# Performance work log

Hardware: AMD Instinct MI355X
Metric: run time of the kernel (lower is better)

Reference implementation:

```python
import jax, jax.numpy as jnp
import numpy as np

SMOOTH = 1.0

def setup_inputs() -> dict:
    key = jax.random.key(0)
    k1, k2 = jax.random.split(key)
    shape = (2, 4, 64, 256, 256)  # [B, organs, D, H, W]
    predict = jax.random.normal(k1, shape, dtype=jnp.float32)
    target = jax.random.uniform(k2, shape, dtype=jnp.float32)
    return {"predict": predict, "target": target}

def reference(predict, target):
    # sigmoid over whole prediction tensor (done once in DiceLoss.forward)
    p = jax.nn.sigmoid(predict)
    B, O, D = p.shape[0], p.shape[1], p.shape[2]
    # BinaryDiceLoss views each [D, H, W] organ slice as (D, H*W):
    pf = p.reshape(B, O, D, -1)
    tf = target.reshape(B, O, D, -1)
    num = jnp.sum(pf * tf, axis=-1)                      # [B, O, D]
    den = jnp.sum(pf, axis=-1) + jnp.sum(tf, axis=-1) + SMOOTH
    dice_loss = 1.0 - 2.0 * num / den                    # [B, O, D]
    # slices with first element == -1 are ignored
    valid = (tf[..., 0] != -1).astype(dice_loss.dtype)   # [B, O, D]
    per_slice_avg = jnp.sum(dice_loss * valid, axis=-1) / jnp.sum(valid, axis=-1)  # [B, O]
    # outer loop averages over all B*4 (b, organ) pairs
    return jnp.mean(per_slice_avg)
```

## Files before the change

kernel.cpp:

```cpp
#include <hip/hip_runtime.h>


constexpr int HW       = 256 * 256;
constexpr int NSLICE   = 2 * 4 * 64;
constexpr int NPAIR    = 2 * 4;
constexpr int THREADS  = 1024;
constexpr int ITERS    = (HW / 4) / THREADS;

__global__ __launch_bounds__(THREADS) void dice_stage1(
    const float* __restrict__ predict,
    const float* __restrict__ target,
    float* __restrict__ ws)
{
    const int slice = blockIdx.x;
    const int tid   = threadIdx.x;
    const size_t base = (size_t)slice * HW;
    const float4* __restrict__ p4 = (const float4*)(predict + base);
    const float4* __restrict__ t4 = (const float4*)(target + base);

    float s_pt = 0.f, s_p = 0.f, s_t = 0.f;
#pragma unroll
    for (int k = 0; k < ITERS; ++k) {
        float4 pv = p4[k * THREADS + tid];
        float4 tv = t4[k * THREADS + tid];
        float e0 = 1.f / (1.f + __expf(-pv.x));
        float e1 = 1.f / (1.f + __expf(-pv.y));
        float e2 = 1.f / (1.f + __expf(-pv.z));
        float e3 = 1.f / (1.f + __expf(-pv.w));
        s_pt += e0 * tv.x;  s_pt += e1 * tv.y;
        s_pt += e2 * tv.z;  s_pt += e3 * tv.w;
        s_p  += (e0 + e1) + (e2 + e3);
        s_t  += (tv.x + tv.y) + (tv.z + tv.w);
    }

#pragma unroll
    for (int off = 32; off > 0; off >>= 1) {
        s_pt += __shfl_down(s_pt, off, 64);
        s_p  += __shfl_down(s_p,  off, 64);
        s_t  += __shfl_down(s_t,  off, 64);
    }

    __shared__ float l_pt[THREADS / 64];
    __shared__ float l_p [THREADS / 64];
    __shared__ float l_t [THREADS / 64];
    const int wave = tid >> 6;
    const int lane = tid & 63;
    if (lane == 0) { l_pt[wave] = s_pt; l_p[wave] = s_p; l_t[wave] = s_t; }
    __syncthreads();

    if (tid == 0) {
        float num = 0.f, sp = 0.f, st = 0.f;
#pragma unroll
        for (int w = 0; w < THREADS / 64; ++w) {
            num += l_pt[w]; sp += l_p[w]; st += l_t[w];
        }
        float den  = sp + st + 1.0f;
        float dice = 1.0f - 2.0f * num / den;
        float valid = (target[base] != -1.0f) ? 1.0f : 0.0f;
        ws[slice]          = dice * valid;
        ws[NSLICE + slice] = valid;
    }
}

__global__ __launch_bounds__(NSLICE) void dice_stage2(
    const float* __restrict__ ws, float* __restrict__ out)
{
    const int tid = threadIdx.x;
    float dv = ws[tid];
    float v  = ws[NSLICE + tid];
#pragma unroll
    for (int off = 32; off > 0; off >>= 1) {
        dv += __shfl_down(dv, off, 64);
        v  += __shfl_down(v,  off, 64);
    }
    __shared__ float pair_avg[NPAIR];
    const int wave = tid >> 6;
    const int lane = tid & 63;
    if (lane == 0) pair_avg[wave] = dv / v;
    __syncthreads();
    if (tid == 0) {
        float s = 0.f;
#pragma unroll
        for (int w = 0; w < NPAIR; ++w) s += pair_avg[w];
        out[0] = s * (1.0f / NPAIR);
    }
}

extern "C" void kernel_launch(void* const* d_in, const int* in_sizes, int n_in,
                              void* d_out, int out_size, void* d_ws, size_t ws_size,
                              hipStream_t stream) {
    const float* predict = (const float*)d_in[0];
    const float* target  = (const float*)d_in[1];
    float* ws  = (float*)d_ws;
    float* out = (float*)d_out;

    dice_stage1<<<NSLICE, THREADS, 0, stream>>>(predict, target, ws);
    dice_stage2<<<1, NSLICE, 0, stream>>>(ws, out);
}
```

Before: 279.2 us.

## Split each slice across four blocks and software-pipeline float4 loads

Stage 1 now launches four 256-thread blocks per slice instead of one 1024-thread block. Each block writes its raw partial sums, and the dice combine plus the validity check move into stage 2. The inner loop prefetches the next batch of four float4 loads before computing the current one, and the product accumulator is split in two to shorten the dependency chain. The goal is more blocks in flight and more memory-level parallelism for a bandwidth-bound reduction. The cost is more register pressure and a slightly larger workspace to reduce in stage 2.

```diff
diff --git a/kernel.cpp b/kernel.cpp
--- a/kernel.cpp
+++ b/kernel.cpp
@@ -1,37 +1,65 @@
 #include <hip/hip_runtime.h>
 
 
-constexpr int HW       = 256 * 256;
-constexpr int NSLICE   = 2 * 4 * 64;
-constexpr int NPAIR    = 2 * 4;
-constexpr int THREADS  = 1024;
-constexpr int ITERS    = (HW / 4) / THREADS;
+constexpr int HW     = 256 * 256;
+constexpr int NSLICE = 2 * 4 * 64;
+constexpr int NPAIR  = 2 * 4;
+constexpr int T      = 256;
+constexpr int CHUNKS_PER_SLICE = 4;
+constexpr int NCHUNK = NSLICE * CHUNKS_PER_SLICE;
+constexpr int CHUNK_ELEMS = HW / CHUNKS_PER_SLICE;
+constexpr int NITER  = CHUNK_ELEMS / 4 / T;
+constexpr int BATCH  = 4;
 
-__global__ __launch_bounds__(THREADS) void dice_stage1(
+
+__global__ __launch_bounds__(T) void dice_stage1(
     const float* __restrict__ predict,
     const float* __restrict__ target,
     float* __restrict__ ws)
 {
-    const int slice = blockIdx.x;
+    const int chunk = blockIdx.x;
     const int tid   = threadIdx.x;
-    const size_t base = (size_t)slice * HW;
+    const size_t base = (size_t)chunk * CHUNK_ELEMS;
     const float4* __restrict__ p4 = (const float4*)(predict + base);
     const float4* __restrict__ t4 = (const float4*)(target + base);
 
-    float s_pt = 0.f, s_p = 0.f, s_t = 0.f;
+    float s_pt0 = 0.f, s_pt1 = 0.f, s_p = 0.f, s_t = 0.f;
+
+    float4 pv[BATCH], tv[BATCH];
 #pragma unroll
-    for (int k = 0; k < ITERS; ++k) {
-        float4 pv = p4[k * THREADS + tid];
-        float4 tv = t4[k * THREADS + tid];
-        float e0 = 1.f / (1.f + __expf(-pv.x));
-        float e1 = 1.f / (1.f + __expf(-pv.y));
-        float e2 = 1.f / (1.f + __expf(-pv.z));
-        float e3 = 1.f / (1.f + __expf(-pv.w));
-        s_pt += e0 * tv.x;  s_pt += e1 * tv.y;
-        s_pt += e2 * tv.z;  s_pt += e3 * tv.w;
-        s_p  += (e0 + e1) + (e2 + e3);
-        s_t  += (tv.x + tv.y) + (tv.z + tv.w);
+    for (int j = 0; j < BATCH; ++j) {
+        pv[j] = p4[j * T + tid];
+        tv[j] = t4[j * T + tid];
     }
+
+#pragma unroll
+    for (int k0 = 0; k0 < NITER; k0 += BATCH) {
+        float4 cp[BATCH], ct[BATCH];
+#pragma unroll
+        for (int j = 0; j < BATCH; ++j) { cp[j] = pv[j]; ct[j] = tv[j]; }
+
+        if (k0 + BATCH < NITER) {
+#pragma unroll
+            for (int j = 0; j < BATCH; ++j) {
+                pv[j] = p4[(k0 + BATCH + j) * T + tid];
+                tv[j] = t4[(k0 + BATCH + j) * T + tid];
+            }
+        }
+
+#pragma unroll
+        for (int j = 0; j < BATCH; ++j) {
+            float e0 = 1.f / (1.f + __expf(-cp[j].x));
+            float e1 = 1.f / (1.f + __expf(-cp[j].y));
+            float e2 = 1.f / (1.f + __expf(-cp[j].z));
+            float e3 = 1.f / (1.f + __expf(-cp[j].w));
+            s_pt0 += e0 * ct[j].x + e1 * ct[j].y;
+            s_pt1 += e2 * ct[j].z + e3 * ct[j].w;
+            s_p   += (e0 + e1) + (e2 + e3);
+            s_t   += (ct[j].x + ct[j].y) + (ct[j].z + ct[j].w);
+        }
+    }
+
+    float s_pt = s_pt0 + s_pt1;
 
 #pragma unroll
     for (int off = 32; off > 0; off >>= 1) {
@@ -40,49 +68,57 @@
         s_t  += __shfl_down(s_t,  off, 64);
     }
 
-    __shared__ float l_pt[THREADS / 64];
-    __shared__ float l_p [THREADS / 64];
-    __shared__ float l_t [THREADS / 64];
+    __shared__ float l_pt[T / 64], l_p[T / 64], l_t[T / 64];
     const int wave = tid >> 6;
     const int lane = tid & 63;
     if (lane == 0) { l_pt[wave] = s_pt; l_p[wave] = s_p; l_t[wave] = s_t; }
     __syncthreads();
 
     if (tid == 0) {
-        float num = 0.f, sp = 0.f, st = 0.f;
+        float a = 0.f, b = 0.f, c = 0.f;
 #pragma unroll
-        for (int w = 0; w < THREADS / 64; ++w) {
-            num += l_pt[w]; sp += l_p[w]; st += l_t[w];
-        }
-        float den  = sp + st + 1.0f;
-        float dice = 1.0f - 2.0f * num / den;
-        float valid = (target[base] != -1.0f) ? 1.0f : 0.0f;
-        ws[slice]          = dice * valid;
-        ws[NSLICE + slice] = valid;
+        for (int w = 0; w < T / 64; ++w) { a += l_pt[w]; b += l_p[w]; c += l_t[w]; }
+        ws[chunk]              = a;
+        ws[NCHUNK + chunk]     = b;
+        ws[2 * NCHUNK + chunk] = c;
     }
 }
 
 __global__ __launch_bounds__(NSLICE) void dice_stage2(
-    const float* __restrict__ ws, float* __restrict__ out)
+    const float* __restrict__ ws,
+    const float* __restrict__ target,
+    float* __restrict__ out)
 {
-    const int tid = threadIdx.x;
-    float dv = ws[tid];
-    float v  = ws[NSLICE + tid];
+    const int s = threadIdx.x;
+    float num = 0.f, sp = 0.f, st = 0.f;
+#pragma unroll
+    for (int c = 0; c < CHUNKS_PER_SLICE; ++c) {
+        const int id = s * CHUNKS_PER_SLICE + c;
+        num += ws[id];
+        sp  += ws[NCHUNK + id];
+        st  += ws[2 * NCHUNK + id];
+    }
+    float den   = sp + st + 1.0f;
+    float dice  = 1.0f - 2.0f * num / den;
+    float valid = (target[(size_t)s * HW] != -1.0f) ? 1.0f : 0.0f;
+
+    float dv = dice * valid;
+    float v  = valid;
 #pragma unroll
     for (int off = 32; off > 0; off >>= 1) {
         dv += __shfl_down(dv, off, 64);
         v  += __shfl_down(v,  off, 64);
     }
     __shared__ float pair_avg[NPAIR];
-    const int wave = tid >> 6;
-    const int lane = tid & 63;
+    const int wave = s >> 6;
+    const int lane = s & 63;
     if (lane == 0) pair_avg[wave] = dv / v;
     __syncthreads();
-    if (tid == 0) {
-        float s = 0.f;
+    if (s == 0) {
+        float acc = 0.f;
 #pragma unroll
-        for (int w = 0; w < NPAIR; ++w) s += pair_avg[w];
-        out[0] = s * (1.0f / NPAIR);
+        for (int w = 0; w < NPAIR; ++w) acc += pair_avg[w];
+        out[0] = acc * (1.0f / NPAIR);
     }
 }
 
@@ -94,6 +130,6 @@
     float* ws  = (float*)d_ws;
     float* out = (float*)d_out;
 
-    dice_stage1<<<NSLICE, THREADS, 0, stream>>>(predict, target, ws);
-    dice_stage2<<<1, NSLICE, 0, stream>>>(ws, out);
+    dice_stage1<<<NCHUNK, T, 0, stream>>>(predict, target, ws);
+    dice_stage2<<<1, NSLICE, 0, stream>>>(ws, target, out);
 }
```

Result: no change. 277.9 us (-0.5%).
